# Performance work log

Hardware: AMD Instinct MI355X
Metric: run time of the kernel (lower is better)

Reference implementation:

```python
import jax, jax.numpy as jnp
import numpy as np

N = 50000
E = 1600000
D_IN = 128
D_OUT = 128


def setup_inputs() -> dict:
    key = jax.random.key(0)
    k1, k2, k3, k4, k5 = jax.random.split(key, 5)
    feature = jax.random.normal(k1, (N, D_IN), dtype=jnp.float32)
    src = jax.random.randint(k2, (E,), 0, N, dtype=jnp.int32)
    dst = jax.random.randint(k3, (E,), 0, N, dtype=jnp.int32)
    # nn.Linear(in_feats, out_feats): weight [out, in], bias [out]
    bound = 1.0 / np.sqrt(D_IN)
    weight = jax.random.uniform(k4, (D_OUT, D_IN), minval=-bound, maxval=bound, dtype=jnp.float32)
    bias = jax.random.uniform(k5, (D_OUT,), minval=-bound, maxval=bound, dtype=jnp.float32)
    return {"feature": feature, "src": src, "dst": dst, "weight": weight, "bias": bias}


def reference(feature, src, dst, weight, bias):
    # message: copy src node feature along each edge; reduce: mean over incoming edges
    msgs = feature[src]                              # [E, D_IN] irregular gather
    summed = jax.ops.segment_sum(msgs, dst, num_segments=N)          # [N, D_IN]
    deg = jax.ops.segment_sum(jnp.ones((E,), dtype=feature.dtype), dst, num_segments=N)  # [N]
    # DGL update_all: zero-in-degree nodes keep their original 'h' (feature)
    mean = summed / jnp.maximum(deg, 1.0)[:, None]
    h = jnp.where((deg > 0)[:, None], mean, feature)  # [N, D_IN]
    out = h @ weight.T + bias                          # Linear
    return jax.nn.relu(out)
```

## Files before the change

kernel.cpp:

```cpp
#include <hip/hip_runtime.h>


#define NN 50000
#define EE 1600000
#define DD 128
#define NSTRIP 3125
#define GSB 196
#define CH2 4096
#define NW2 391
#define NCNT (GSB * NW2)
#define NSA 75
#define WCAP 12288

typedef __attribute__((ext_vector_type(8))) short bf16x8;
typedef __attribute__((ext_vector_type(8))) unsigned short u16x8;
typedef __attribute__((ext_vector_type(4))) float f32x4;

static __device__ __forceinline__ short f2bf(float f) {
  union { float f; unsigned u; } x; x.f = f;
  unsigned r = (x.u + 0x7FFF + ((x.u >> 16) & 1)) >> 16;
  return (short)(r & 0xFFFF);
}

__global__ __launch_bounds__(256) void p1b(
    const int* __restrict__ dst, int* __restrict__ cnt2) {
  __shared__ int cnt[4][GSB];
  const int wv = threadIdx.x >> 6, lane = threadIdx.x & 63;
  const int w = blockIdx.x * 4 + wv;
  const bool act = (w < NW2);
  for (int i = lane; i < GSB; i += 64) cnt[wv][i] = 0;
  __syncthreads();
  if (act) {
    const int base = w * CH2;
#pragma unroll 4
    for (int it = 0; it < 16; ++it) {
      int e0 = base + it * 256 + lane * 4;
      if (e0 < EE) {
        int4 d4 = *(const int4*)(dst + e0);
        atomicAdd(&cnt[wv][((unsigned)d4.x) >> 8], 1);
        atomicAdd(&cnt[wv][((unsigned)d4.y) >> 8], 1);
        atomicAdd(&cnt[wv][((unsigned)d4.z) >> 8], 1);
        atomicAdd(&cnt[wv][((unsigned)d4.w) >> 8], 1);
      }
    }
  }
  __syncthreads();
  if (act) {
    for (int i = lane; i < GSB; i += 64) cnt2[i * NW2 + w] = cnt[wv][i];
  }
}

__global__ __launch_bounds__(1024) void sA_bsum(
    const int* __restrict__ in, int* __restrict__ bsum, int n) {
  __shared__ int ws[16];
  int i = blockIdx.x * 1024 + threadIdx.x;
  int v = (i < n) ? in[i] : 0;
#pragma unroll
  for (int d = 1; d < 64; d <<= 1) v += __shfl_xor(v, d, 64);
  int wv = threadIdx.x >> 6, lane = threadIdx.x & 63;
  if (lane == 0) ws[wv] = v;
  __syncthreads();
  if (threadIdx.x == 0) {
    int s = 0;
#pragma unroll
    for (int k = 0; k < 16; ++k) s += ws[k];
    bsum[blockIdx.x] = s;
  }
}

__global__ __launch_bounds__(1024) void p2_scan(
    const int* __restrict__ in, int* __restrict__ out, int n) {
  __shared__ int ws[16];
  __shared__ int s_off;
  const int wv = threadIdx.x >> 6, lane = threadIdx.x & 63;
  if (threadIdx.x == 0) s_off = 0;
  __syncthreads();
  for (int base = 0; base < n; base += 1024) {
    int i = base + threadIdx.x;
    int v = (i < n) ? in[i] : 0;
    int x = v;
#pragma unroll
    for (int d = 1; d < 64; d <<= 1) { int t = __shfl_up(x, d, 64); if (lane >= d) x += t; }
    if (lane == 63) ws[wv] = x;
    __syncthreads();
    if (threadIdx.x < 16) {
      int w = ws[threadIdx.x];
#pragma unroll
      for (int d = 1; d < 16; d <<= 1) { int t = __shfl_up(w, d, 16); if (threadIdx.x >= d) w += t; }
      ws[threadIdx.x] = w;
    }
    __syncthreads();
    int off = s_off + ((wv == 0) ? 0 : ws[wv - 1]);
    if (i < n) out[i] = off + x - v;
    __syncthreads();
    if (threadIdx.x == 0) s_off += ws[15];
    __syncthreads();
  }
}

__global__ __launch_bounds__(1024) void sC_apply(
    int* __restrict__ data, const int* __restrict__ bsum, int n) {
  __shared__ int ws[16];
  int i = blockIdx.x * 1024 + threadIdx.x;
  int wv = threadIdx.x >> 6, lane = threadIdx.x & 63;
  int v = (i < n) ? data[i] : 0;
  int x = v;
#pragma unroll
  for (int d = 1; d < 64; d <<= 1) { int t = __shfl_up(x, d, 64); if (lane >= d) x += t; }
  if (lane == 63) ws[wv] = x;
  __syncthreads();
  if (threadIdx.x < 16) {
    int w = ws[threadIdx.x];
#pragma unroll
    for (int d = 1; d < 16; d <<= 1) { int t = __shfl_up(w, d, 16); if (threadIdx.x >= d) w += t; }
    ws[threadIdx.x] = w;
  }
  __syncthreads();
  int off = bsum[blockIdx.x] + ((wv == 0) ? 0 : ws[wv - 1]);
  if (i < n) data[i] = off + x - v;
}

__global__ __launch_bounds__(256) void p3b(
    const int* __restrict__ src, const int* __restrict__ dst,
    const int* __restrict__ off2, unsigned int* __restrict__ ss) {
  __shared__ int cur[4][GSB];
  const int wv = threadIdx.x >> 6, lane = threadIdx.x & 63;
  const int w = blockIdx.x * 4 + wv;
  const bool act = (w < NW2);
  if (act) {
    for (int i = lane; i < GSB; i += 64) cur[wv][i] = off2[i * NW2 + w];
  }
  __syncthreads();
  if (act) {
    const int base = w * CH2;
#pragma unroll 2
    for (int it = 0; it < 16; ++it) {
      int e0 = base + it * 256 + lane * 4;
      if (e0 < EE) {
        int4 s4 = *(const int4*)(src + e0);
        int4 d4 = *(const int4*)(dst + e0);
        {
          int p = atomicAdd(&cur[wv][((unsigned)d4.x) >> 8], 1);
          ss[p] = (((unsigned)d4.x) << 16) | (unsigned)s4.x;
        }
        {
          int p = atomicAdd(&cur[wv][((unsigned)d4.y) >> 8], 1);
          ss[p] = (((unsigned)d4.y) << 16) | (unsigned)s4.y;
        }
        {
          int p = atomicAdd(&cur[wv][((unsigned)d4.z) >> 8], 1);
          ss[p] = (((unsigned)d4.z) << 16) | (unsigned)s4.z;
        }
        {
          int p = atomicAdd(&cur[wv][((unsigned)d4.w) >> 8], 1);
          ss[p] = (((unsigned)d4.w) << 16) | (unsigned)s4.w;
        }
      }
    }
  }
}

__global__ __launch_bounds__(1024) void fillL2(
    const unsigned int* __restrict__ ss, const int* __restrict__ off2,
    int* __restrict__ csr, int* __restrict__ row_start) {
  __shared__ int win[WCAP];
  __shared__ int cur[256];
  __shared__ int rs[257];
  __shared__ int wsum2[4];
  const int g    = blockIdx.x;
  const int lo   = g * 256;
  const int nloc = (NN - lo < 256) ? (NN - lo) : 256;
  const int ebase = off2[g * NW2];
  const int eend  = (g < GSB - 1) ? off2[(g + 1) * NW2] : EE;
  const int T = eend - ebase;

  if (threadIdx.x < 256) cur[threadIdx.x] = 0;
  __syncthreads();

  for (int e = ebase + threadIdx.x; e < eend; e += 1024) {
    atomicAdd(&cur[(ss[e] >> 16) & 255], 1);
  }
  __syncthreads();

  int x = 0;
  if (threadIdx.x < 256) {
    const int lane = threadIdx.x & 63;
    x = cur[threadIdx.x];
#pragma unroll
    for (int d = 1; d < 64; d <<= 1) { int t = __shfl_up(x, d, 64); if (lane >= d) x += t; }
    if (lane == 63) wsum2[threadIdx.x >> 6] = x;
  }
  __syncthreads();
  if (threadIdx.x < 256) {
    const int wv2 = threadIdx.x >> 6;
    int pre = 0;
#pragma unroll
    for (int k = 0; k < 4; ++k) pre += (k < wv2) ? wsum2[k] : 0;
    rs[threadIdx.x + 1] = pre + x;
    if (threadIdx.x == 0) rs[0] = 0;
    cur[threadIdx.x] = 0;
  }
  __syncthreads();

  if (threadIdx.x <= nloc) row_start[lo + threadIdx.x] = ebase + rs[threadIdx.x];

  if (T <= WCAP) {
    for (int e = ebase + threadIdx.x; e < eend; e += 1024) {
      unsigned pe = ss[e];
      int li = (pe >> 16) & 255;
      int p = atomicAdd(&cur[li], 1);
      win[rs[li] + p] = (int)(pe & 0xFFFFu);
    }
    __syncthreads();
    for (int i = threadIdx.x; i < T; i += 1024) csr[ebase + i] = win[i];
  } else {
    for (int e = ebase + threadIdx.x; e < eend; e += 1024) {
      unsigned pe = ss[e];
      int li = (pe >> 16) & 255;
      int p = atomicAdd(&cur[li], 1);
      csr[ebase + rs[li] + p] = (int)(pe & 0xFFFFu);
    }
  }
}

__global__ __launch_bounds__(256) void feat2bf_kernel(
    const float* __restrict__ feature, unsigned short* __restrict__ fb) {
  int i = blockIdx.x * 256 + threadIdx.x;
  if (i < NN * DD / 4) {
    float4 v = ((const float4*)feature)[i];
    short4 o;
    o.x = f2bf(v.x); o.y = f2bf(v.y); o.z = f2bf(v.z); o.w = f2bf(v.w);
    ((short4*)fb)[i] = o;
  }
}

__global__ __launch_bounds__(256) void aggregate_bf16(
    const unsigned short* __restrict__ fb,
    const int* __restrict__ row_start,
    const int* __restrict__ csr_src,
    unsigned short* __restrict__ hb) {
  const int wave = threadIdx.x >> 6;
  const int lane = threadIdx.x & 63;
  int n = blockIdx.x * 4 + wave;
  if (n >= NN) return;

  const int start = row_start[n];
  const int end   = row_start[n + 1];
  const int deg   = end - start;
  const int q  = lane >> 4;
  const int sl = lane & 15;

  const u16x8* fp = (const u16x8*)fb;
  float acc[8];
#pragma unroll
  for (int j = 0; j < 8; ++j) acc[j] = 0.f;

#pragma unroll 4
  for (int e = start + q; e < end; e += 4) {
    int s = csr_src[e];
    u16x8 v = fp[(size_t)s * 16 + sl];
#pragma unroll
    for (int j = 0; j < 8; ++j) {
      union { unsigned u; float f; } c; c.u = ((unsigned)v[j]) << 16;
      acc[j] += c.f;
    }
  }
#pragma unroll
  for (int j = 0; j < 8; ++j) {
    acc[j] += __shfl_xor(acc[j], 16, 64);
    acc[j] += __shfl_xor(acc[j], 32, 64);
  }

  if (q == 0) {
    u16x8 hv;
    if (deg > 0) {
      float inv = 1.0f / (float)deg;
#pragma unroll
      for (int j = 0; j < 8; ++j) hv[j] = (unsigned short)f2bf(acc[j] * inv);
    } else {
      hv = fp[(size_t)n * 16 + sl];
    }
    ((u16x8*)hb)[(size_t)n * 16 + sl] = hv;
  }
}

__global__ __launch_bounds__(256) void mfma_gemm2(
    const short* __restrict__ hb,
    const float* __restrict__ weight,
    const float* __restrict__ bias,
    float* __restrict__ out) {
  __shared__ bf16x8 wfrag[2048];
  __shared__ float  bias_l[DD];

#pragma unroll
  for (int k = 0; k < 8; ++k) {
    int idx  = threadIdx.x * 8 + k;
    int ln   = idx & 63;
    int ct   = idx >> 6;
    int c    = ct >> 2;
    int t    = ct & 3;
    const float* wp = weight + (c * 16 + (ln & 15)) * DD + t * 32 + (ln >> 4) * 8;
    float4 w0 = *(const float4*)(wp);
    float4 w1 = *(const float4*)(wp + 4);
    bf16x8 b;
    b[0] = f2bf(w0.x); b[1] = f2bf(w0.y); b[2] = f2bf(w0.z); b[3] = f2bf(w0.w);
    b[4] = f2bf(w1.x); b[5] = f2bf(w1.y); b[6] = f2bf(w1.z); b[7] = f2bf(w1.w);
    wfrag[idx] = b;
  }
  if (threadIdx.x < DD) bias_l[threadIdx.x] = bias[threadIdx.x];
  __syncthreads();

  const int wave = threadIdx.x >> 6;
  const int lane = threadIdx.x & 63;
  const int r  = lane & 15;
  const int g  = lane >> 4;

#pragma unroll
  for (int s = 0; s < 2; ++s) {
    const int strip = blockIdx.x * 8 + wave * 2 + s;
    if (strip >= NSTRIP) continue;
    const int m0 = strip * 16;

    bf16x8 Af[4];
#pragma unroll
    for (int t = 0; t < 4; ++t) {
      Af[t] = *(const bf16x8*)(hb + (size_t)(m0 + r) * DD + t * 32 + g * 8);
    }

#pragma unroll
    for (int c = 0; c < 8; ++c) {
      f32x4 acc = {0.f, 0.f, 0.f, 0.f};
#pragma unroll
      for (int t = 0; t < 4; ++t) {
        acc = __builtin_amdgcn_mfma_f32_16x16x32_bf16(Af[t], wfrag[(c * 4 + t) * 64 + lane], acc, 0, 0, 0);
      }
      const float b = bias_l[c * 16 + r];
#pragma unroll
      for (int q = 0; q < 4; ++q) {
        int row = m0 + g * 4 + q;
        float v = acc[q] + b;
        out[(size_t)row * DD + c * 16 + r] = v > 0.f ? v : 0.f;
      }
    }
  }
}

extern "C" void kernel_launch(void* const* d_in, const int* in_sizes, int n_in,
                              void* d_out, int out_size, void* d_ws, size_t ws_size,
                              hipStream_t stream) {
  const float* feature = (const float*)d_in[0];
  const int*   src     = (const int*)d_in[1];
  const int*   dst     = (const int*)d_in[2];
  const float* weight  = (const float*)d_in[3];
  const float* bias    = (const float*)d_in[4];
  float* out = (float*)d_out;

  int* cnt2      = (int*)d_ws;
  int* bsum      = cnt2 + 76640;
  int* row_start = bsum + 80;
  unsigned short* hb = (unsigned short*)(cnt2 + 126724);

  unsigned int* ss = (unsigned int*)d_out;
  int* csr = (int*)d_out + EE;
  unsigned short* fb = (unsigned short*)((int*)d_out + 2 * EE);

  feat2bf_kernel<<<(NN * DD / 4 + 255) / 256, 256, 0, stream>>>(feature, fb);
  p1b<<<98, 256, 0, stream>>>(dst, cnt2);
  sA_bsum<<<NSA, 1024, 0, stream>>>(cnt2, bsum, NCNT);
  p2_scan<<<1, 1024, 0, stream>>>(bsum, bsum, NSA);
  sC_apply<<<NSA, 1024, 0, stream>>>(cnt2, bsum, NCNT);
  p3b<<<98, 256, 0, stream>>>(src, dst, cnt2, ss);
  fillL2<<<GSB, 1024, 0, stream>>>(ss, cnt2, csr, row_start);
  aggregate_bf16<<<(NN + 3) / 4, 256, 0, stream>>>(fb, row_start, csr, hb);
  mfma_gemm2<<<(NSTRIP + 7) / 8, 256, 0, stream>>>((const short*)hb, weight, bias, out);
}
```

Before: 109.3 us.

## Fuse histogram with bf16 conversion and fold the scan into the scatter kernel

The dst histogram and the feature-to-bf16 conversion now run in one launch, using separate block ranges. The three-kernel scan (block sums, single-block scan, apply) is removed. Each scatter block instead recomputes its own per-bucket prefix offsets directly from the count matrix and writes the bucket starts for the fill kernel. This cuts four launches and their serialization gaps, at the cost of each scatter block redundantly reading the whole 196x391 count matrix. The aggregation loop unroll also goes from 4 to 8.

```diff
diff --git a/kernel.cpp b/kernel.cpp
--- a/kernel.cpp
+++ b/kernel.cpp
@@ -8,8 +8,8 @@
 #define GSB 196
 #define CH2 4096
 #define NW2 391
-#define NCNT (GSB * NW2)
-#define NSA 75
+#define NPBLK 98
+#define NFB 6250
 #define WCAP 12288
 
 typedef __attribute__((ext_vector_type(8))) short bf16x8;
@@ -22,116 +22,103 @@
   return (short)(r & 0xFFFF);
 }
 
-__global__ __launch_bounds__(256) void p1b(
-    const int* __restrict__ dst, int* __restrict__ cnt2) {
-  __shared__ int cnt[4][GSB];
+__global__ __launch_bounds__(256) void k1(
+    const int* __restrict__ dst, int* __restrict__ cnt2,
+    const float* __restrict__ feature, unsigned short* __restrict__ fb) {
+  if (blockIdx.x < NPBLK) {
+    __shared__ int cnt[4][GSB];
+    const int wv = threadIdx.x >> 6, lane = threadIdx.x & 63;
+    const int w = blockIdx.x * 4 + wv;
+    const bool act = (w < NW2);
+    for (int i = lane; i < GSB; i += 64) cnt[wv][i] = 0;
+    __syncthreads();
+    if (act) {
+      const int base = w * CH2;
+#pragma unroll 4
+      for (int it = 0; it < 16; ++it) {
+        int e0 = base + it * 256 + lane * 4;
+        if (e0 < EE) {
+          int4 d4 = *(const int4*)(dst + e0);
+          atomicAdd(&cnt[wv][((unsigned)d4.x) >> 8], 1);
+          atomicAdd(&cnt[wv][((unsigned)d4.y) >> 8], 1);
+          atomicAdd(&cnt[wv][((unsigned)d4.z) >> 8], 1);
+          atomicAdd(&cnt[wv][((unsigned)d4.w) >> 8], 1);
+        }
+      }
+    }
+    __syncthreads();
+    if (act) {
+      for (int i = lane; i < GSB; i += 64) cnt2[i * NW2 + w] = cnt[wv][i];
+    }
+  } else {
+    int i = (blockIdx.x - NPBLK) * 256 + threadIdx.x;
+    if (i < NN * DD / 4) {
+      float4 v = ((const float4*)feature)[i];
+      short4 o;
+      o.x = f2bf(v.x); o.y = f2bf(v.y); o.z = f2bf(v.z); o.w = f2bf(v.w);
+      ((short4*)fb)[i] = o;
+    }
+  }
+}
+
+__global__ __launch_bounds__(256) void p3c(
+    const int* __restrict__ src, const int* __restrict__ dst,
+    const int* __restrict__ cnt2, unsigned int* __restrict__ ss,
+    int* __restrict__ Pi_g) {
+  __shared__ int cur[4][GSB];
+  __shared__ int tarr[GSB];
+  __shared__ int pw[4][GSB];
+  __shared__ int wsum[4];
+  const int w0 = blockIdx.x * 4;
+
+  for (int i = threadIdx.x; i < GSB; i += 256) {
+    const int* row = cnt2 + i * NW2;
+    int p = 0;
+    for (int w = 0; w < w0; ++w) p += row[w];
+    int p0 = p;
+    int p1 = p0 + ((w0 + 0 < NW2) ? row[w0 + 0] : 0);
+    int p2 = p1 + ((w0 + 1 < NW2) ? row[w0 + 1] : 0);
+    int p3 = p2 + ((w0 + 2 < NW2) ? row[w0 + 2] : 0);
+    int t = p3;
+    for (int w = w0 + 3; w < NW2; ++w) t += row[w];
+    tarr[i] = t;
+    pw[0][i] = p0; pw[1][i] = p1; pw[2][i] = p2; pw[3][i] = p3;
+  }
+  __syncthreads();
+
+  {
+    const int lane = threadIdx.x & 63;
+    const int wv = threadIdx.x >> 6;
+    int v = (threadIdx.x < GSB) ? tarr[threadIdx.x] : 0;
+    int x = v;
+#pragma unroll
+    for (int d = 1; d < 64; d <<= 1) { int t = __shfl_up(x, d, 64); if (lane >= d) x += t; }
+    if (lane == 63) wsum[wv] = x;
+    __syncthreads();
+    int pre = 0;
+#pragma unroll
+    for (int k = 0; k < 4; ++k) pre += (k < wv) ? wsum[k] : 0;
+    if (threadIdx.x < GSB) {
+      int Pi = pre + x - v;
+      tarr[threadIdx.x] = Pi;
+      Pi_g[threadIdx.x] = Pi;
+      if (threadIdx.x == 0) Pi_g[GSB] = EE;
+    }
+  }
+  __syncthreads();
+
+  for (int i = threadIdx.x; i < GSB; i += 256) {
+    int Pi = tarr[i];
+    cur[0][i] = Pi + pw[0][i];
+    cur[1][i] = Pi + pw[1][i];
+    cur[2][i] = Pi + pw[2][i];
+    cur[3][i] = Pi + pw[3][i];
+  }
+  __syncthreads();
+
   const int wv = threadIdx.x >> 6, lane = threadIdx.x & 63;
-  const int w = blockIdx.x * 4 + wv;
-  const bool act = (w < NW2);
-  for (int i = lane; i < GSB; i += 64) cnt[wv][i] = 0;
-  __syncthreads();
-  if (act) {
-    const int base = w * CH2;
-#pragma unroll 4
-    for (int it = 0; it < 16; ++it) {
-      int e0 = base + it * 256 + lane * 4;
-      if (e0 < EE) {
-        int4 d4 = *(const int4*)(dst + e0);
-        atomicAdd(&cnt[wv][((unsigned)d4.x) >> 8], 1);
-        atomicAdd(&cnt[wv][((unsigned)d4.y) >> 8], 1);
-        atomicAdd(&cnt[wv][((unsigned)d4.z) >> 8], 1);
-        atomicAdd(&cnt[wv][((unsigned)d4.w) >> 8], 1);
-      }
-    }
-  }
-  __syncthreads();
-  if (act) {
-    for (int i = lane; i < GSB; i += 64) cnt2[i * NW2 + w] = cnt[wv][i];
-  }
-}
-
-__global__ __launch_bounds__(1024) void sA_bsum(
-    const int* __restrict__ in, int* __restrict__ bsum, int n) {
-  __shared__ int ws[16];
-  int i = blockIdx.x * 1024 + threadIdx.x;
-  int v = (i < n) ? in[i] : 0;
-#pragma unroll
-  for (int d = 1; d < 64; d <<= 1) v += __shfl_xor(v, d, 64);
-  int wv = threadIdx.x >> 6, lane = threadIdx.x & 63;
-  if (lane == 0) ws[wv] = v;
-  __syncthreads();
-  if (threadIdx.x == 0) {
-    int s = 0;
-#pragma unroll
-    for (int k = 0; k < 16; ++k) s += ws[k];
-    bsum[blockIdx.x] = s;
-  }
-}
-
-__global__ __launch_bounds__(1024) void p2_scan(
-    const int* __restrict__ in, int* __restrict__ out, int n) {
-  __shared__ int ws[16];
-  __shared__ int s_off;
-  const int wv = threadIdx.x >> 6, lane = threadIdx.x & 63;
-  if (threadIdx.x == 0) s_off = 0;
-  __syncthreads();
-  for (int base = 0; base < n; base += 1024) {
-    int i = base + threadIdx.x;
-    int v = (i < n) ? in[i] : 0;
-    int x = v;
-#pragma unroll
-    for (int d = 1; d < 64; d <<= 1) { int t = __shfl_up(x, d, 64); if (lane >= d) x += t; }
-    if (lane == 63) ws[wv] = x;
-    __syncthreads();
-    if (threadIdx.x < 16) {
-      int w = ws[threadIdx.x];
-#pragma unroll
-      for (int d = 1; d < 16; d <<= 1) { int t = __shfl_up(w, d, 16); if (threadIdx.x >= d) w += t; }
-      ws[threadIdx.x] = w;
-    }
-    __syncthreads();
-    int off = s_off + ((wv == 0) ? 0 : ws[wv - 1]);
-    if (i < n) out[i] = off + x - v;
-    __syncthreads();
-    if (threadIdx.x == 0) s_off += ws[15];
-    __syncthreads();
-  }
-}
-
-__global__ __launch_bounds__(1024) void sC_apply(
-    int* __restrict__ data, const int* __restrict__ bsum, int n) {
-  __shared__ int ws[16];
-  int i = blockIdx.x * 1024 + threadIdx.x;
-  int wv = threadIdx.x >> 6, lane = threadIdx.x & 63;
-  int v = (i < n) ? data[i] : 0;
-  int x = v;
-#pragma unroll
-  for (int d = 1; d < 64; d <<= 1) { int t = __shfl_up(x, d, 64); if (lane >= d) x += t; }
-  if (lane == 63) ws[wv] = x;
-  __syncthreads();
-  if (threadIdx.x < 16) {
-    int w = ws[threadIdx.x];
-#pragma unroll
-    for (int d = 1; d < 16; d <<= 1) { int t = __shfl_up(w, d, 16); if (threadIdx.x >= d) w += t; }
-    ws[threadIdx.x] = w;
-  }
-  __syncthreads();
-  int off = bsum[blockIdx.x] + ((wv == 0) ? 0 : ws[wv - 1]);
-  if (i < n) data[i] = off + x - v;
-}
-
-__global__ __launch_bounds__(256) void p3b(
-    const int* __restrict__ src, const int* __restrict__ dst,
-    const int* __restrict__ off2, unsigned int* __restrict__ ss) {
-  __shared__ int cur[4][GSB];
-  const int wv = threadIdx.x >> 6, lane = threadIdx.x & 63;
-  const int w = blockIdx.x * 4 + wv;
-  const bool act = (w < NW2);
-  if (act) {
-    for (int i = lane; i < GSB; i += 64) cur[wv][i] = off2[i * NW2 + w];
-  }
-  __syncthreads();
-  if (act) {
+  const int w = w0 + wv;
+  if (w < NW2) {
     const int base = w * CH2;
 #pragma unroll 2
     for (int it = 0; it < 16; ++it) {
@@ -160,8 +147,8 @@
   }
 }
 
-__global__ __launch_bounds__(1024) void fillL2(
-    const unsigned int* __restrict__ ss, const int* __restrict__ off2,
+__global__ __launch_bounds__(1024) void fillL3(
+    const unsigned int* __restrict__ ss, const int* __restrict__ Pi_g,
     int* __restrict__ csr, int* __restrict__ row_start) {
   __shared__ int win[WCAP];
   __shared__ int cur[256];
@@ -170,8 +157,8 @@
   const int g    = blockIdx.x;
   const int lo   = g * 256;
   const int nloc = (NN - lo < 256) ? (NN - lo) : 256;
-  const int ebase = off2[g * NW2];
-  const int eend  = (g < GSB - 1) ? off2[(g + 1) * NW2] : EE;
+  const int ebase = Pi_g[g];
+  const int eend  = Pi_g[g + 1];
   const int T = eend - ebase;
 
   if (threadIdx.x < 256) cur[threadIdx.x] = 0;
@@ -220,17 +207,6 @@
       int p = atomicAdd(&cur[li], 1);
       csr[ebase + rs[li] + p] = (int)(pe & 0xFFFFu);
     }
-  }
-}
-
-__global__ __launch_bounds__(256) void feat2bf_kernel(
-    const float* __restrict__ feature, unsigned short* __restrict__ fb) {
-  int i = blockIdx.x * 256 + threadIdx.x;
-  if (i < NN * DD / 4) {
-    float4 v = ((const float4*)feature)[i];
-    short4 o;
-    o.x = f2bf(v.x); o.y = f2bf(v.y); o.z = f2bf(v.z); o.w = f2bf(v.w);
-    ((short4*)fb)[i] = o;
   }
 }
 
@@ -255,7 +231,7 @@
 #pragma unroll
   for (int j = 0; j < 8; ++j) acc[j] = 0.f;
 
-#pragma unroll 4
+#pragma unroll 8
   for (int e = start + q; e < end; e += 4) {
     int s = csr_src[e];
     u16x8 v = fp[(size_t)s * 16 + sl];
@@ -356,21 +332,17 @@
   float* out = (float*)d_out;
 
   int* cnt2      = (int*)d_ws;
-  int* bsum      = cnt2 + 76640;
-  int* row_start = bsum + 80;
-  unsigned short* hb = (unsigned short*)(cnt2 + 126724);
+  int* Pi_g      = cnt2 + 76640;
+  int* row_start = Pi_g + 200;
+  unsigned short* hb = (unsigned short*)(cnt2 + 126844);
 
   unsigned int* ss = (unsigned int*)d_out;
   int* csr = (int*)d_out + EE;
   unsigned short* fb = (unsigned short*)((int*)d_out + 2 * EE);
 
-  feat2bf_kernel<<<(NN * DD / 4 + 255) / 256, 256, 0, stream>>>(feature, fb);
-  p1b<<<98, 256, 0, stream>>>(dst, cnt2);
-  sA_bsum<<<NSA, 1024, 0, stream>>>(cnt2, bsum, NCNT);
-  p2_scan<<<1, 1024, 0, stream>>>(bsum, bsum, NSA);
-  sC_apply<<<NSA, 1024, 0, stream>>>(cnt2, bsum, NCNT);
-  p3b<<<98, 256, 0, stream>>>(src, dst, cnt2, ss);
-  fillL2<<<GSB, 1024, 0, stream>>>(ss, cnt2, csr, row_start);
+  k1<<<NPBLK + NFB, 256, 0, stream>>>(dst, cnt2, feature, fb);
+  p3c<<<NPBLK, 256, 0, stream>>>(src, dst, cnt2, ss, Pi_g);
+  fillL3<<<GSB, 1024, 0, stream>>>(ss, Pi_g, csr, row_start);
   aggregate_bf16<<<(NN + 3) / 4, 256, 0, stream>>>(fb, row_start, csr, hb);
   mfma_gemm2<<<(NSTRIP + 7) / 8, 256, 0, stream>>>((const short*)hb, weight, bias, out);
 }
```

After: 163.8 us. +49.8%, slower.
